# Optimization experiments

Hardware: AMD Instinct MI355X
Metric: run time of the kernel (lower is better)

The kernel has to match this reference:

```python
import jax, jax.numpy as jnp
import numpy as np

B, S, E, H = 2, 2048, 1024, 16
HD = E // H


def setup_inputs() -> dict:
    key = jax.random.key(0)
    ks = jax.random.split(key, 5)
    scale = 1.0 / np.sqrt(E)
    return {
        "x": jax.random.normal(ks[0], (B, S, E), dtype=jnp.float32),
        "Wq": jax.random.normal(ks[1], (H, HD, E), dtype=jnp.float32) * scale,
        "Wk": jax.random.normal(ks[2], (H, HD, E), dtype=jnp.float32) * scale,
        "Wv": jax.random.normal(ks[3], (H, HD, E), dtype=jnp.float32) * scale,
        "Wo": jax.random.normal(ks[4], (E, E), dtype=jnp.float32) * scale,
    }


def reference(x, Wq, Wk, Wv, Wo):
    # Batched per-head projections: torch Linear y = x @ W.T, W: [head_dim, E]
    q = jnp.einsum("bse,hde->bshd", x, Wq)  # [B,S,H,HD]
    k = jnp.einsum("bse,hde->bshd", x, Wk)
    v = jnp.einsum("bse,hde->bshd", x, Wv)
    # Scaled dot-product attention; original scales by sqrt(head_dim)
    scores = jnp.einsum("bqhd,bkhd->bhqk", q, k) / jnp.sqrt(jnp.float32(HD))
    attn = jax.nn.softmax(scores, axis=-1)  # [B,H,S,S]
    out_h = jnp.einsum("bhqk,bkhd->bqhd", attn, v)  # [B,S,H,HD]
    out_cat = out_h.reshape(x.shape[0], x.shape[1], -1)  # concat heads -> [B,S,E]
    return out_cat @ Wo.T
```

## Files before the change

### kernel.cpp

```cpp
#include <hip/hip_runtime.h>
#include <hip/hip_bf16.h>

typedef unsigned short u16;
typedef unsigned int u32;
typedef __attribute__((ext_vector_type(4))) float f32x4;
typedef __attribute__((ext_vector_type(8))) short short8;
typedef __attribute__((ext_vector_type(8))) unsigned short u16x8;
typedef __attribute__((ext_vector_type(4))) unsigned short u16x4;
typedef __attribute__((ext_vector_type(2))) unsigned int u32x2;

#define BATCH 2
#define SEQ   2048
#define EMB   1024
#define NH    16
#define HD    64

__device__ inline u16 f2bf(float f) {
    unsigned u = __builtin_bit_cast(unsigned, f);
    unsigned r = u + 0x7FFFu + ((u >> 16) & 1u);
    return (u16)(r >> 16);
}

__device__ inline float fexp2(float x) {
    float r;
    asm("v_exp_f32 %0, %1" : "=v"(r) : "v"(x));
    return r;
}

__device__ inline void gload16(const void* g, void* l) {
    __builtin_amdgcn_global_load_lds(
        (const __attribute__((address_space(1))) unsigned int*)g,
        (__attribute__((address_space(3))) unsigned int*)l, 16, 0, 0);
}

__global__ __launch_bounds__(256) void convert_all(
    const float* __restrict__ x,
    const float* __restrict__ Wq, const float* __restrict__ Wk, const float* __restrict__ Wv,
    u16* __restrict__ Xb, u16* __restrict__ Wqkv)
{
    const long gidx = (long)blockIdx.x * 2048 + (long)threadIdx.x * 8;
    const float* src;
    u16* dst;
    if (gidx < 4194304L) {
        src = x + gidx; dst = Xb + gidx;
    } else {
        const long r = gidx - 4194304L;
        const int w = (int)(r >> 20);
        const long off = r & 1048575L;
        src = (w == 0 ? Wq : w == 1 ? Wk : Wv) + off;
        dst = Wqkv + r;
    }
    f32x4 a = *(const f32x4*)src;
    f32x4 b = *(const f32x4*)(src + 4);
    u16x8 o;
    #pragma unroll
    for (int j = 0; j < 4; ++j) { o[j] = f2bf(a[j]); o[4 + j] = f2bf(b[j]); }
    *(u16x8*)dst = o;
}

__global__ __launch_bounds__(256) void convert_wo(
    const float* __restrict__ Wo, u16* __restrict__ Wob)
{
    const long gidx = (long)blockIdx.x * 2048 + (long)threadIdx.x * 8;
    f32x4 a = *(const f32x4*)(Wo + gidx);
    f32x4 b = *(const f32x4*)(Wo + gidx + 4);
    u16x8 o;
    #pragma unroll
    for (int j = 0; j < 4; ++j) { o[j] = f2bf(a[j]); o[4 + j] = f2bf(b[j]); }
    *(u16x8*)(Wob + gidx) = o;
}

__global__ __launch_bounds__(512, 2) void gemm256(
    const u16* __restrict__ A, const u16* __restrict__ Bb,
    u16* __restrict__ Qo, u16* __restrict__ Ko, u16* __restrict__ VTo)
{
    __shared__ u16 As[2][256 * 64];
    __shared__ u16 Bs[2][256 * 64];

    const int tid = threadIdx.x;
    const int lane = tid & 63;
    const int wid = tid >> 6;
    const int lr = lane & 15;
    const int lg = lane >> 4;
    const int wr = wid >> 2;
    const int wc = wid & 3;

    const int lin = blockIdx.y * 16 + blockIdx.x;
    const int swz = (lin & 7) * 24 + (lin >> 3);
    const int m0 = (swz & 15) * 256;
    const int n0 = (swz >> 4) * 256;

    const int grow = lane >> 3;
    const int schunk = ((lane & 7) ^ grow) << 4;

    auto issueTile = [&](int kt, int buf) {
        const int k0b = kt * 128;
        #pragma unroll
        for (int i = 0; i < 4; ++i) {
            const int row = i * 64 + wid * 8 + grow;
            gload16((const char*)A + (size_t)(m0 + row) * 2048 + k0b + schunk,
                    (char*)As[buf] + i * 8192 + wid * 1024);
            gload16((const char*)Bb + (size_t)(n0 + row) * 2048 + k0b + schunk,
                    (char*)Bs[buf] + i * 8192 + wid * 1024);
        }
    };

    issueTile(0, 0);
    issueTile(1, 1);

    f32x4 acc[8][4] = {};
    const int rsw = (lr & 7);

    for (int t = 0; t < 16; ++t) {
        if (t < 15) { asm volatile("s_waitcnt vmcnt(8)" ::: "memory"); }
        else        { asm volatile("s_waitcnt vmcnt(0)" ::: "memory"); }
        __builtin_amdgcn_sched_barrier(0);
        __builtin_amdgcn_s_barrier();
        __builtin_amdgcn_sched_barrier(0);

        const u16* Ac = As[t & 1];
        const u16* Bc = Bs[t & 1];

        short8 a[4][2], b0[2][2], b1[2][2];

        #pragma unroll
        for (int fi = 0; fi < 4; ++fi)
            #pragma unroll
            for (int ks = 0; ks < 2; ++ks)
                a[fi][ks] = *(const short8*)((const char*)Ac + (wr * 128 + fi * 16 + lr) * 128
                                             + (((ks * 4 + lg) ^ rsw) << 4));
        #pragma unroll
        for (int fj = 0; fj < 2; ++fj)
            #pragma unroll
            for (int ks = 0; ks < 2; ++ks)
                b0[fj][ks] = *(const short8*)((const char*)Bc + (wc * 64 + fj * 16 + lr) * 128
                                              + (((ks * 4 + lg) ^ rsw) << 4));
        __builtin_amdgcn_s_setprio(1);
        #pragma unroll
        for (int fi = 0; fi < 4; ++fi)
            #pragma unroll
            for (int fj = 0; fj < 2; ++fj)
                #pragma unroll
                for (int ks = 0; ks < 2; ++ks)
                    acc[fi][fj] = __builtin_amdgcn_mfma_f32_16x16x32_bf16(a[fi][ks], b0[fj][ks], acc[fi][fj], 0, 0, 0);
        __builtin_amdgcn_s_setprio(0);

        #pragma unroll
        for (int fj = 0; fj < 2; ++fj)
            #pragma unroll
            for (int ks = 0; ks < 2; ++ks)
                b1[fj][ks] = *(const short8*)((const char*)Bc + (wc * 64 + (fj + 2) * 16 + lr) * 128
                                              + (((ks * 4 + lg) ^ rsw) << 4));
        __builtin_amdgcn_s_setprio(1);
        #pragma unroll
        for (int fi = 0; fi < 4; ++fi)
            #pragma unroll
            for (int fj = 0; fj < 2; ++fj)
                #pragma unroll
                for (int ks = 0; ks < 2; ++ks)
                    acc[fi][fj + 2] = __builtin_amdgcn_mfma_f32_16x16x32_bf16(a[fi][ks], b1[fj][ks], acc[fi][fj + 2], 0, 0, 0);
        __builtin_amdgcn_s_setprio(0);

        #pragma unroll
        for (int fi = 0; fi < 4; ++fi)
            #pragma unroll
            for (int ks = 0; ks < 2; ++ks)
                a[fi][ks] = *(const short8*)((const char*)Ac + (wr * 128 + (fi + 4) * 16 + lr) * 128
                                             + (((ks * 4 + lg) ^ rsw) << 4));
        __builtin_amdgcn_s_setprio(1);
        #pragma unroll
        for (int fi = 0; fi < 4; ++fi)
            #pragma unroll
            for (int fj = 0; fj < 2; ++fj)
                #pragma unroll
                for (int ks = 0; ks < 2; ++ks)
                    acc[fi + 4][fj + 2] = __builtin_amdgcn_mfma_f32_16x16x32_bf16(a[fi][ks], b1[fj][ks], acc[fi + 4][fj + 2], 0, 0, 0);
        __builtin_amdgcn_s_setprio(0);

        __builtin_amdgcn_s_setprio(1);
        #pragma unroll
        for (int fi = 0; fi < 4; ++fi)
            #pragma unroll
            for (int fj = 0; fj < 2; ++fj)
                #pragma unroll
                for (int ks = 0; ks < 2; ++ks)
                    acc[fi + 4][fj] = __builtin_amdgcn_mfma_f32_16x16x32_bf16(a[fi][ks], b0[fj][ks], acc[fi + 4][fj], 0, 0, 0);
        __builtin_amdgcn_s_setprio(0);

        __builtin_amdgcn_sched_barrier(0);
        __builtin_amdgcn_s_barrier();
        __builtin_amdgcn_sched_barrier(0);
        if (t + 2 < 16) issueTile(t + 2, t & 1);
    }

    const int w = n0 >> 10;
    const float qs = (w == 0) ? 0.125f * 1.44269504f : 1.0f;
    const int mb = m0 + wr * 128;
    const int nb = n0 + wc * 64;
    #pragma unroll
    for (int fi = 0; fi < 8; ++fi) {
        #pragma unroll
        for (int fj = 0; fj < 4; ++fj) {
            const int m = mb + fi * 16 + lg * 4;
            const int nn = (nb + fj * 16 + lr) & 1023;
            const int h = nn >> 6, d = nn & 63;
            const int bb = m >> 11, s = m & 2047;
            const size_t bh = (size_t)(bb * NH + h);
            if (w == 2) {
                u16x4 v;
                #pragma unroll
                for (int i = 0; i < 4; ++i) v[i] = f2bf(acc[fi][fj][i]);
                *(u16x4*)&VTo[(bh * HD + d) * SEQ + s] = v;
            } else {
                u16* P = (w == 0) ? Qo : Ko;
                #pragma unroll
                for (int i = 0; i < 4; ++i)
                    P[(bh * SEQ + s + i) * HD + d] = f2bf(acc[fi][fj][i] * qs);
            }
        }
    }
}

__global__ __launch_bounds__(256) void gemm_out(
    const u16* __restrict__ A, const u16* __restrict__ Bb, float* __restrict__ Fo)
{
    __shared__ u16 As[2][128 * 64];
    __shared__ u16 Bs[2][128 * 64];

    const int tid = threadIdx.x;
    const int m0 = blockIdx.x * 128;
    const int n0 = blockIdx.y * 128;

    const int lane = tid & 63;
    const int lr = lane & 15;
    const int lg = lane >> 4;
    const int wid = tid >> 6;
    const int wm = wid >> 1, wn = wid & 1;

    const int grow = lane >> 3;
    const int gcolb = ((lane & 7) ^ grow) << 4;
    const int rswz = (lr & 7);

    f32x4 acc[4][4] = {};

    auto issue = [&](int kt, int buf) {
        const int k0b = kt * 128;
        #pragma unroll
        for (int t = 0; t < 4; ++t) {
            const int row = (wid * 4 + t) * 8 + grow;
            gload16((const char*)A + (size_t)(m0 + row) * 2048 + k0b + gcolb,
                    (char*)As[buf] + (wid * 4 + t) * 1024);
            gload16((const char*)Bb + (size_t)(n0 + row) * 2048 + k0b + gcolb,
                    (char*)Bs[buf] + (wid * 4 + t) * 1024);
        }
    };

    issue(0, 0);
    issue(1, 1);

    for (int kt = 0; kt < 16; ++kt) {
        if (kt < 15) { asm volatile("s_waitcnt vmcnt(8)" ::: "memory"); }
        else         { asm volatile("s_waitcnt vmcnt(0)" ::: "memory"); }
        __builtin_amdgcn_sched_barrier(0);
        __builtin_amdgcn_s_barrier();
        __builtin_amdgcn_sched_barrier(0);

        const u16* Ac = As[kt & 1];
        const u16* Bc = Bs[kt & 1];
        #pragma unroll
        for (int kk = 0; kk < 2; ++kk) {
            short8 a[4], b[4];
            #pragma unroll
            for (int i = 0; i < 4; ++i)
                a[i] = *(const short8*)((const char*)Ac + (wm * 64 + i * 16 + lr) * 128
                                        + (((kk * 4 + lg) ^ rswz) << 4));
            #pragma unroll
            for (int i = 0; i < 4; ++i)
                b[i] = *(const short8*)((const char*)Bc + (wn * 64 + i * 16 + lr) * 128
                                        + (((kk * 4 + lg) ^ rswz) << 4));
            #pragma unroll
            for (int mi = 0; mi < 4; ++mi)
                #pragma unroll
                for (int ni = 0; ni < 4; ++ni)
                    acc[mi][ni] = __builtin_amdgcn_mfma_f32_16x16x32_bf16(a[mi], b[ni], acc[mi][ni], 0, 0, 0);
        }

        __builtin_amdgcn_sched_barrier(0);
        __builtin_amdgcn_s_barrier();
        __builtin_amdgcn_sched_barrier(0);
        if (kt + 2 < 16) issue(kt + 2, kt & 1);
    }

    const int mb = m0 + wm * 64;
    const int nb = n0 + wn * 64;
    #pragma unroll
    for (int mi = 0; mi < 4; ++mi)
        #pragma unroll
        for (int ni = 0; ni < 4; ++ni) {
            const int m = mb + mi * 16 + lg * 4;
            const int n = nb + ni * 16 + lr;
            #pragma unroll
            for (int i = 0; i < 4; ++i)
                Fo[(size_t)(m + i) * EMB + n] = acc[mi][ni][i];
        }
}

__global__ __launch_bounds__(512) void attn_fwd(
    const u16* __restrict__ Q, const u16* __restrict__ K,
    const u16* __restrict__ VT, u16* __restrict__ Cat)
{
    __shared__ u16 Ks[2][64 * 64];
    __shared__ u16 Vs[2][80 * 64];
    __shared__ u16 PT[8][16 * 72];

    const int tid = threadIdx.x;
    const int lane = tid & 63;
    const int lr = lane & 15;
    const int lg = lane >> 4;
    const int wid = tid >> 6;

    const int lin = blockIdx.y * 16 + blockIdx.x;
    const int swz = (lin & 7) * 64 + (lin >> 3);
    const int qt = swz & 15;
    const int bh = swz >> 4;
    const int b = bh >> 4, h = bh & 15;

    if (tid < 128) {
        const int row = 64 + (tid >> 3), sl = tid & 7;
        u16x8 ones;
        #pragma unroll
        for (int j = 0; j < 8; ++j) ones[j] = 0x3F80;
        *(u16x8*)((char*)Vs[0] + row * 128 + ((sl ^ (row & 7)) << 4)) = ones;
        *(u16x8*)((char*)Vs[1] + row * 128 + ((sl ^ (row & 7)) << 4)) = ones;
    }
    asm volatile("s_waitcnt lgkmcnt(0)" ::: "memory");

    const u16* Qg = Q + ((size_t)bh * SEQ + qt * 128 + wid * 16 + lr) * HD;
    short8 qf[2];
    qf[0] = *(const short8*)(Qg + lg * 8);
    qf[1] = *(const short8*)(Qg + 32 + lg * 8);

    float m = -1e30f;
    f32x4 accO[5] = {};

    const u16* Kg = K + (size_t)bh * SEQ * HD;
    const u16* Vg = VT + (size_t)bh * HD * SEQ;

    const int srow = lane >> 3;
    const int schunk = ((lane & 7) ^ srow) << 4;

    auto issueKV = [&](int nt, int buf) {
        const int kv0 = nt * 64;
        const int krow = wid * 8 + srow;
        gload16((const char*)Kg + (size_t)(kv0 + krow) * 128 + schunk,
                (char*)Ks[buf] + wid * 1024);
        gload16((const char*)Vg + (size_t)krow * (SEQ * 2) + kv0 * 2 + schunk,
                (char*)Vs[buf] + wid * 1024);
    };

    issueKV(0, 0);
    issueKV(1, 1);

    const int NT = SEQ / 64;
    for (int nt = 0; nt < NT; ++nt) {
        const int cur = nt & 1;
        if (nt < NT - 1) { asm volatile("s_waitcnt vmcnt(2)" ::: "memory"); }
        else             { asm volatile("s_waitcnt vmcnt(0)" ::: "memory"); }
        __builtin_amdgcn_sched_barrier(0);
        __builtin_amdgcn_s_barrier();
        __builtin_amdgcn_sched_barrier(0);

        f32x4 st[4] = {};
        #pragma unroll
        for (int kk = 0; kk < 2; ++kk) {
            const short8 qv = qf[kk];
            #pragma unroll
            for (int c = 0; c < 4; ++c) {
                const short8 kf = *(const short8*)((const char*)Ks[cur] + (c * 16 + lr) * 128
                                                   + (((kk * 4 + lg) ^ (lr & 7)) << 4));
                st[c] = __builtin_amdgcn_mfma_f32_16x16x32_bf16(kf, qv, st[c], 0, 0, 0);
            }
        }

        float mx = fmaxf(
            fmaxf(fmaxf(fmaxf(st[0][0], st[0][1]), fmaxf(st[0][2], st[0][3])),
                  fmaxf(fmaxf(st[1][0], st[1][1]), fmaxf(st[1][2], st[1][3]))),
            fmaxf(fmaxf(fmaxf(st[2][0], st[2][1]), fmaxf(st[2][2], st[2][3])),
                  fmaxf(fmaxf(st[3][0], st[3][1]), fmaxf(st[3][2], st[3][3]))));
        mx = fmaxf(mx, __shfl_xor(mx, 16));
        mx = fmaxf(mx, __shfl_xor(mx, 32));
        if (!__all(mx - m <= 11.5f)) {
            const float nm = fmaxf(m, mx);
            const float corr = fexp2(m - nm);
            m = nm;
            #pragma unroll
            for (int dc = 0; dc < 5; ++dc)
                accO[dc] *= corr;
        }
        #pragma unroll
        for (int c = 0; c < 4; ++c)
            #pragma unroll
            for (int i = 0; i < 4; ++i)
                st[c][i] = fexp2(st[c][i] - m);

        #pragma unroll
        for (int c = 0; c < 4; ++c) {
            u32 w0, w1;
            asm("v_cvt_pk_bf16_f32 %0, %1, %2" : "=v"(w0) : "v"(st[c][0]), "v"(st[c][1]));
            asm("v_cvt_pk_bf16_f32 %0, %1, %2" : "=v"(w1) : "v"(st[c][2]), "v"(st[c][3]));
            u32x2 pk; pk[0] = w0; pk[1] = w1;
            *(u32x2*)&PT[wid][lr * 72 + c * 16 + lg * 4] = pk;
        }
        asm volatile("s_waitcnt lgkmcnt(0)" ::: "memory");
        __builtin_amdgcn_sched_barrier(0);

        #pragma unroll
        for (int kk = 0; kk < 2; ++kk) {
            const short8 pf = *(const short8*)&PT[wid][lr * 72 + kk * 32 + lg * 8];
            #pragma unroll
            for (int dc = 0; dc < 5; ++dc) {
                const short8 vf = *(const short8*)((const char*)Vs[cur] + (dc * 16 + lr) * 128
                                                   + (((kk * 4 + lg) ^ (lr & 7)) << 4));
                accO[dc] = __builtin_amdgcn_mfma_f32_16x16x32_bf16(vf, pf, accO[dc], 0, 0, 0);
            }
        }

        __builtin_amdgcn_sched_barrier(0);
        __builtin_amdgcn_s_barrier();
        __builtin_amdgcn_sched_barrier(0);
        if (nt + 2 < NT) issueKV(nt + 2, cur);
    }

    const float invl = 1.f / accO[4][0];
    const int qs = qt * 128 + wid * 16 + lr;
    u16* ob = Cat + (size_t)b * SEQ * EMB + (size_t)qs * EMB + h * HD;
    #pragma unroll
    for (int dc = 0; dc < 4; ++dc) {
        u16x4 o;
        #pragma unroll
        for (int i = 0; i < 4; ++i) o[i] = f2bf(accO[dc][i] * invl);
        *(u16x4*)&ob[dc * 16 + lg * 4] = o;
    }
}

extern "C" void kernel_launch(void* const* d_in, const int* in_sizes, int n_in,
                              void* d_out, int out_size, void* d_ws, size_t ws_size,
                              hipStream_t stream) {
    const float* x  = (const float*)d_in[0];
    const float* Wq = (const float*)d_in[1];
    const float* Wk = (const float*)d_in[2];
    const float* Wv = (const float*)d_in[3];
    const float* Wo = (const float*)d_in[4];
    float* out = (float*)d_out;

    u16* Xb   = (u16*)d_out;
    u16* Wqkv = (u16*)d_out + (size_t)4 * 1048576;

    char* ws = (char*)d_ws;
    u16* Qb  = (u16*)(ws);
    u16* Kb  = (u16*)(ws + (size_t)8  * 1048576);
    u16* VTb = (u16*)(ws + (size_t)16 * 1048576);
    u16* Cat = (u16*)(ws + (size_t)24 * 1048576);
    u16* Wob = Qb;

    convert_all<<<3584, 256, 0, stream>>>(x, Wq, Wk, Wv, Xb, Wqkv);

    dim3 g1(4096 / 256, 3072 / 256);
    gemm256<<<g1, 512, 0, stream>>>(Xb, Wqkv, Qb, Kb, VTb);

    dim3 g2(SEQ / 128, BATCH * NH);
    attn_fwd<<<g2, 512, 0, stream>>>(Qb, Kb, VTb, Cat);

    convert_wo<<<512, 256, 0, stream>>>(Wo, Wob);
    dim3 g3(4096 / 128, 1024 / 128);
    gemm_out<<<g3, 256, 0, stream>>>(Cat, Wob, out);
}
```

Measured before the change: 126.2 us.

## Software-pipeline PV matmul behind next QK tile; swizzle output GEMM blocks

The attention loop now runs the P·V MFMAs for the previous KV tile right after the current tile's QK^T MFMAs. This lets softmax exp work and the two MFMA chains overlap, and drops one workgroup barrier per iteration. V staging grows to four LDS buffers so the delayed PV read does not collide with incoming prefetches, at the cost of extra LDS and one epilogue PV step. Separately, the output projection GEMM remaps block indices with a grouped swizzle, so blocks running at the same time share A/B tiles in L2.

```diff
diff --git a/kernel.cpp b/kernel.cpp
--- a/kernel.cpp
+++ b/kernel.cpp
@@ -228,8 +228,11 @@
     __shared__ u16 Bs[2][128 * 64];
 
     const int tid = threadIdx.x;
-    const int m0 = blockIdx.x * 128;
-    const int n0 = blockIdx.y * 128;
+
+    const int lin = blockIdx.y * 32 + blockIdx.x;
+    const int swz = (lin & 7) * 32 + (lin >> 3);
+    const int m0 = (swz & 31) * 128;
+    const int n0 = (swz >> 5) * 128;
 
     const int lane = tid & 63;
     const int lr = lane & 15;
@@ -310,7 +313,7 @@
     const u16* __restrict__ VT, u16* __restrict__ Cat)
 {
     __shared__ u16 Ks[2][64 * 64];
-    __shared__ u16 Vs[2][80 * 64];
+    __shared__ u16 Vs[4][80 * 64];
     __shared__ u16 PT[8][16 * 72];
 
     const int tid = threadIdx.x;
@@ -330,8 +333,10 @@
         u16x8 ones;
         #pragma unroll
         for (int j = 0; j < 8; ++j) ones[j] = 0x3F80;
-        *(u16x8*)((char*)Vs[0] + row * 128 + ((sl ^ (row & 7)) << 4)) = ones;
-        *(u16x8*)((char*)Vs[1] + row * 128 + ((sl ^ (row & 7)) << 4)) = ones;
+        const int off = row * 128 + ((sl ^ (row & 7)) << 4);
+        #pragma unroll
+        for (int bf = 0; bf < 4; ++bf)
+            *(u16x8*)((char*)Vs[bf] + off) = ones;
     }
     asm volatile("s_waitcnt lgkmcnt(0)" ::: "memory");
 
@@ -349,17 +354,17 @@
     const int srow = lane >> 3;
     const int schunk = ((lane & 7) ^ srow) << 4;
 
-    auto issueKV = [&](int nt, int buf) {
+    auto issueKV = [&](int nt) {
         const int kv0 = nt * 64;
         const int krow = wid * 8 + srow;
         gload16((const char*)Kg + (size_t)(kv0 + krow) * 128 + schunk,
-                (char*)Ks[buf] + wid * 1024);
+                (char*)Ks[nt & 1] + wid * 1024);
         gload16((const char*)Vg + (size_t)krow * (SEQ * 2) + kv0 * 2 + schunk,
-                (char*)Vs[buf] + wid * 1024);
+                (char*)Vs[nt & 3] + wid * 1024);
     };
 
-    issueKV(0, 0);
-    issueKV(1, 1);
+    issueKV(0);
+    issueKV(1);
 
     const int NT = SEQ / 64;
     for (int nt = 0; nt < NT; ++nt) {
@@ -379,6 +384,20 @@
                 const short8 kf = *(const short8*)((const char*)Ks[cur] + (c * 16 + lr) * 128
                                                    + (((kk * 4 + lg) ^ (lr & 7)) << 4));
                 st[c] = __builtin_amdgcn_mfma_f32_16x16x32_bf16(kf, qv, st[c], 0, 0, 0);
+            }
+        }
+
+        if (nt > 0) {
+            const char* Vp = (const char*)Vs[(nt - 1) & 3];
+            #pragma unroll
+            for (int kk = 0; kk < 2; ++kk) {
+                const short8 pf = *(const short8*)&PT[wid][lr * 72 + kk * 32 + lg * 8];
+                #pragma unroll
+                for (int dc = 0; dc < 5; ++dc) {
+                    const short8 vf = *(const short8*)(Vp + (dc * 16 + lr) * 128
+                                                       + (((kk * 4 + lg) ^ (lr & 7)) << 4));
+                    accO[dc] = __builtin_amdgcn_mfma_f32_16x16x32_bf16(vf, pf, accO[dc], 0, 0, 0);
+                }
             }
         }
 
@@ -414,21 +433,23 @@
         asm volatile("s_waitcnt lgkmcnt(0)" ::: "memory");
         __builtin_amdgcn_sched_barrier(0);
 
+        __builtin_amdgcn_s_barrier();
+        __builtin_amdgcn_sched_barrier(0);
+        if (nt + 2 < NT) issueKV(nt + 2);
+    }
+
+    {
+        const char* Vp = (const char*)Vs[(NT - 1) & 3];
         #pragma unroll
         for (int kk = 0; kk < 2; ++kk) {
             const short8 pf = *(const short8*)&PT[wid][lr * 72 + kk * 32 + lg * 8];
             #pragma unroll
             for (int dc = 0; dc < 5; ++dc) {
-                const short8 vf = *(const short8*)((const char*)Vs[cur] + (dc * 16 + lr) * 128
+                const short8 vf = *(const short8*)(Vp + (dc * 16 + lr) * 128
                                                    + (((kk * 4 + lg) ^ (lr & 7)) << 4));
                 accO[dc] = __builtin_amdgcn_mfma_f32_16x16x32_bf16(vf, pf, accO[dc], 0, 0, 0);
             }
         }
-
-        __builtin_amdgcn_sched_barrier(0);
-        __builtin_amdgcn_s_barrier();
-        __builtin_amdgcn_sched_barrier(0);
-        if (nt + 2 < NT) issueKV(nt + 2, cur);
     }
 
     const float invl = 1.f / accO[4][0];
```

Result: no change. 128.1 us (+1.6%).

## Rewrite attention with 32x32 MFMA and register-resident P via permlane swaps

Applied to the files above, without the earlier changes.

The attention kernel moves from 16x16x32 to 32x32x16 bf16 MFMA with 32 query rows per wave and 256 per block. The probability tile is kept in registers using v_permlane32_swap instead of going through a shared-memory PT buffer. The row sum is now computed explicitly rather than through an extra ones-row in V. The output GEMM also gets a block-index swizzle for L2 locality. The aim is to cut LDS traffic and waits and raise MFMA efficiency, at the cost of more registers per wave and half as many attention blocks.

```diff
diff --git a/kernel.cpp b/kernel.cpp
--- a/kernel.cpp
+++ b/kernel.cpp
@@ -4,10 +4,11 @@
 typedef unsigned short u16;
 typedef unsigned int u32;
 typedef __attribute__((ext_vector_type(4))) float f32x4;
+typedef __attribute__((ext_vector_type(16))) float f32x16;
 typedef __attribute__((ext_vector_type(8))) short short8;
 typedef __attribute__((ext_vector_type(8))) unsigned short u16x8;
 typedef __attribute__((ext_vector_type(4))) unsigned short u16x4;
-typedef __attribute__((ext_vector_type(2))) unsigned int u32x2;
+typedef __attribute__((ext_vector_type(4))) unsigned int u32x4;
 
 #define BATCH 2
 #define SEQ   2048
@@ -32,6 +33,27 @@
         (const __attribute__((address_space(1))) unsigned int*)g,
         (__attribute__((address_space(3))) unsigned int*)l, 16, 0, 0);
 }
+
+__device__ inline short8 mk8(u32 a, u32 b, u32 c, u32 d) {
+    u32x4 t; t[0] = a; t[1] = b; t[2] = c; t[3] = d;
+    return __builtin_bit_cast(short8, t);
+}
+
+#define PACK_ST(st, w0,w1,w2,w3,w4,w5,w6,w7)                                   \
+  {                                                                            \
+    asm("v_cvt_pk_bf16_f32 %0, %1, %2" : "=v"(w0) : "v"(st[0]),  "v"(st[1]));  \
+    asm("v_cvt_pk_bf16_f32 %0, %1, %2" : "=v"(w1) : "v"(st[2]),  "v"(st[3]));  \
+    asm("v_cvt_pk_bf16_f32 %0, %1, %2" : "=v"(w2) : "v"(st[4]),  "v"(st[5]));  \
+    asm("v_cvt_pk_bf16_f32 %0, %1, %2" : "=v"(w3) : "v"(st[6]),  "v"(st[7]));  \
+    asm("v_permlane32_swap_b32 %0, %1" : "+v"(w0), "+v"(w2));                  \
+    asm("v_permlane32_swap_b32 %0, %1" : "+v"(w1), "+v"(w3));                  \
+    asm("v_cvt_pk_bf16_f32 %0, %1, %2" : "=v"(w4) : "v"(st[8]),  "v"(st[9]));  \
+    asm("v_cvt_pk_bf16_f32 %0, %1, %2" : "=v"(w5) : "v"(st[10]), "v"(st[11])); \
+    asm("v_cvt_pk_bf16_f32 %0, %1, %2" : "=v"(w6) : "v"(st[12]), "v"(st[13])); \
+    asm("v_cvt_pk_bf16_f32 %0, %1, %2" : "=v"(w7) : "v"(st[14]), "v"(st[15])); \
+    asm("v_permlane32_swap_b32 %0, %1" : "+v"(w4), "+v"(w6));                  \
+    asm("v_permlane32_swap_b32 %0, %1" : "+v"(w5), "+v"(w7));                  \
+  }
 
 __global__ __launch_bounds__(256) void convert_all(
     const float* __restrict__ x,
@@ -228,8 +250,11 @@
     __shared__ u16 Bs[2][128 * 64];
 
     const int tid = threadIdx.x;
-    const int m0 = blockIdx.x * 128;
-    const int n0 = blockIdx.y * 128;
+
+    const int lin = blockIdx.y * 32 + blockIdx.x;
+    const int swz = (lin & 7) * 32 + (lin >> 3);
+    const int m0 = (swz & 31) * 128;
+    const int n0 = (swz >> 5) * 128;
 
     const int lane = tid & 63;
     const int lr = lane & 15;
@@ -310,38 +335,28 @@
     const u16* __restrict__ VT, u16* __restrict__ Cat)
 {
     __shared__ u16 Ks[2][64 * 64];
-    __shared__ u16 Vs[2][80 * 64];
-    __shared__ u16 PT[8][16 * 72];
+    __shared__ u16 Vs[2][64 * 64];
 
     const int tid = threadIdx.x;
     const int lane = tid & 63;
-    const int lr = lane & 15;
-    const int lg = lane >> 4;
     const int wid = tid >> 6;
-
-    const int lin = blockIdx.y * 16 + blockIdx.x;
-    const int swz = (lin & 7) * 64 + (lin >> 3);
-    const int qt = swz & 15;
-    const int bh = swz >> 4;
+    const int lq = lane & 31;
+    const int hi = lane >> 5;
+
+    const int lin = blockIdx.y * 8 + blockIdx.x;
+    const int swz = (lin & 7) * 32 + (lin >> 3);
+    const int qt = swz & 7;
+    const int bh = swz >> 3;
     const int b = bh >> 4, h = bh & 15;
 
-    if (tid < 128) {
-        const int row = 64 + (tid >> 3), sl = tid & 7;
-        u16x8 ones;
-        #pragma unroll
-        for (int j = 0; j < 8; ++j) ones[j] = 0x3F80;
-        *(u16x8*)((char*)Vs[0] + row * 128 + ((sl ^ (row & 7)) << 4)) = ones;
-        *(u16x8*)((char*)Vs[1] + row * 128 + ((sl ^ (row & 7)) << 4)) = ones;
-    }
-    asm volatile("s_waitcnt lgkmcnt(0)" ::: "memory");
-
-    const u16* Qg = Q + ((size_t)bh * SEQ + qt * 128 + wid * 16 + lr) * HD;
-    short8 qf[2];
-    qf[0] = *(const short8*)(Qg + lg * 8);
-    qf[1] = *(const short8*)(Qg + 32 + lg * 8);
-
-    float m = -1e30f;
-    f32x4 accO[5] = {};
+    const u16* Qg = Q + ((size_t)bh * SEQ + qt * 256 + wid * 32 + lq) * HD;
+    short8 qf[4];
+    #pragma unroll
+    for (int ks = 0; ks < 4; ++ks)
+        qf[ks] = *(const short8*)((const char*)Qg + ks * 32 + hi * 16);
+
+    float m = -1e30f, l = 0.f;
+    f32x16 ot0 = {}, ot1 = {};
 
     const u16* Kg = K + (size_t)bh * SEQ * HD;
     const u16* Vg = VT + (size_t)bh * HD * SEQ;
@@ -349,18 +364,19 @@
     const int srow = lane >> 3;
     const int schunk = ((lane & 7) ^ srow) << 4;
 
-    auto issueKV = [&](int nt, int buf) {
+    auto issueKV = [&](int nt) {
         const int kv0 = nt * 64;
         const int krow = wid * 8 + srow;
         gload16((const char*)Kg + (size_t)(kv0 + krow) * 128 + schunk,
-                (char*)Ks[buf] + wid * 1024);
+                (char*)Ks[nt & 1] + wid * 1024);
         gload16((const char*)Vg + (size_t)krow * (SEQ * 2) + kv0 * 2 + schunk,
-                (char*)Vs[buf] + wid * 1024);
+                (char*)Vs[nt & 1] + wid * 1024);
     };
 
-    issueKV(0, 0);
-    issueKV(1, 1);
-
+    issueKV(0);
+    issueKV(1);
+
+    const int rsw = (lq & 7);
     const int NT = SEQ / 64;
     for (int nt = 0; nt < NT; ++nt) {
         const int cur = nt & 1;
@@ -370,76 +386,77 @@
         __builtin_amdgcn_s_barrier();
         __builtin_amdgcn_sched_barrier(0);
 
-        f32x4 st[4] = {};
-        #pragma unroll
-        for (int kk = 0; kk < 2; ++kk) {
-            const short8 qv = qf[kk];
-            #pragma unroll
-            for (int c = 0; c < 4; ++c) {
-                const short8 kf = *(const short8*)((const char*)Ks[cur] + (c * 16 + lr) * 128
-                                                   + (((kk * 4 + lg) ^ (lr & 7)) << 4));
-                st[c] = __builtin_amdgcn_mfma_f32_16x16x32_bf16(kf, qv, st[c], 0, 0, 0);
-            }
-        }
-
-        float mx = fmaxf(
-            fmaxf(fmaxf(fmaxf(st[0][0], st[0][1]), fmaxf(st[0][2], st[0][3])),
-                  fmaxf(fmaxf(st[1][0], st[1][1]), fmaxf(st[1][2], st[1][3]))),
-            fmaxf(fmaxf(fmaxf(st[2][0], st[2][1]), fmaxf(st[2][2], st[2][3])),
-                  fmaxf(fmaxf(st[3][0], st[3][1]), fmaxf(st[3][2], st[3][3]))));
-        mx = fmaxf(mx, __shfl_xor(mx, 16));
+        f32x16 st0 = {}, st1 = {};
+        #pragma unroll
+        for (int ks = 0; ks < 4; ++ks) {
+            const int co = ((ks * 2 + hi) ^ rsw) << 4;
+            const short8 kf0 = *(const short8*)((const char*)Ks[cur] + lq * 128 + co);
+            const short8 kf1 = *(const short8*)((const char*)Ks[cur] + (32 + lq) * 128 + co);
+            st0 = __builtin_amdgcn_mfma_f32_32x32x16_bf16(kf0, qf[ks], st0, 0, 0, 0);
+            st1 = __builtin_amdgcn_mfma_f32_32x32x16_bf16(kf1, qf[ks], st1, 0, 0, 0);
+        }
+
+        float mx = st0[0];
+        #pragma unroll
+        for (int i = 1; i < 16; ++i) mx = fmaxf(mx, st0[i]);
+        #pragma unroll
+        for (int i = 0; i < 16; ++i) mx = fmaxf(mx, st1[i]);
         mx = fmaxf(mx, __shfl_xor(mx, 32));
         if (!__all(mx - m <= 11.5f)) {
             const float nm = fmaxf(m, mx);
             const float corr = fexp2(m - nm);
             m = nm;
-            #pragma unroll
-            for (int dc = 0; dc < 5; ++dc)
-                accO[dc] *= corr;
-        }
-        #pragma unroll
-        for (int c = 0; c < 4; ++c)
-            #pragma unroll
-            for (int i = 0; i < 4; ++i)
-                st[c][i] = fexp2(st[c][i] - m);
-
-        #pragma unroll
-        for (int c = 0; c < 4; ++c) {
-            u32 w0, w1;
-            asm("v_cvt_pk_bf16_f32 %0, %1, %2" : "=v"(w0) : "v"(st[c][0]), "v"(st[c][1]));
-            asm("v_cvt_pk_bf16_f32 %0, %1, %2" : "=v"(w1) : "v"(st[c][2]), "v"(st[c][3]));
-            u32x2 pk; pk[0] = w0; pk[1] = w1;
-            *(u32x2*)&PT[wid][lr * 72 + c * 16 + lg * 4] = pk;
-        }
-        asm volatile("s_waitcnt lgkmcnt(0)" ::: "memory");
-        __builtin_amdgcn_sched_barrier(0);
-
-        #pragma unroll
-        for (int kk = 0; kk < 2; ++kk) {
-            const short8 pf = *(const short8*)&PT[wid][lr * 72 + kk * 32 + lg * 8];
-            #pragma unroll
-            for (int dc = 0; dc < 5; ++dc) {
-                const short8 vf = *(const short8*)((const char*)Vs[cur] + (dc * 16 + lr) * 128
-                                                   + (((kk * 4 + lg) ^ (lr & 7)) << 4));
-                accO[dc] = __builtin_amdgcn_mfma_f32_16x16x32_bf16(vf, pf, accO[dc], 0, 0, 0);
-            }
-        }
-
-        __builtin_amdgcn_sched_barrier(0);
-        __builtin_amdgcn_s_barrier();
-        __builtin_amdgcn_sched_barrier(0);
-        if (nt + 2 < NT) issueKV(nt + 2, cur);
-    }
-
-    const float invl = 1.f / accO[4][0];
-    const int qs = qt * 128 + wid * 16 + lr;
-    u16* ob = Cat + (size_t)b * SEQ * EMB + (size_t)qs * EMB + h * HD;
-    #pragma unroll
-    for (int dc = 0; dc < 4; ++dc) {
-        u16x4 o;
-        #pragma unroll
-        for (int i = 0; i < 4; ++i) o[i] = f2bf(accO[dc][i] * invl);
-        *(u16x4*)&ob[dc * 16 + lg * 4] = o;
+            l *= corr;
+            #pragma unroll
+            for (int i = 0; i < 16; ++i) { ot0[i] *= corr; ot1[i] *= corr; }
+        }
+        float rs = 0.f;
+        #pragma unroll
+        for (int i = 0; i < 16; ++i) {
+            st0[i] = fexp2(st0[i] - m); rs += st0[i];
+            st1[i] = fexp2(st1[i] - m); rs += st1[i];
+        }
+        rs += __shfl_xor(rs, 32);
+        l += rs;
+
+        u32 a0, a1, a2, a3, a4, a5, a6, a7;
+        u32 c0, c1, c2, c3, c4, c5, c6, c7;
+        PACK_ST(st0, a0, a1, a2, a3, a4, a5, a6, a7);
+        PACK_ST(st1, c0, c1, c2, c3, c4, c5, c6, c7);
+        const short8 pf0 = mk8(a0, a1, a2, a3);
+        const short8 pf1 = mk8(a4, a5, a6, a7);
+        const short8 pf2 = mk8(c0, c1, c2, c3);
+        const short8 pf3 = mk8(c4, c5, c6, c7);
+
+        #pragma unroll
+        for (int ks = 0; ks < 4; ++ks) {
+            const short8 pf = (ks == 0) ? pf0 : (ks == 1) ? pf1 : (ks == 2) ? pf2 : pf3;
+            const int co = ((ks * 2 + hi) ^ rsw) << 4;
+            const short8 vf0 = *(const short8*)((const char*)Vs[cur] + lq * 128 + co);
+            const short8 vf1 = *(const short8*)((const char*)Vs[cur] + (32 + lq) * 128 + co);
+            ot0 = __builtin_amdgcn_mfma_f32_32x32x16_bf16(vf0, pf, ot0, 0, 0, 0);
+            ot1 = __builtin_amdgcn_mfma_f32_32x32x16_bf16(vf1, pf, ot1, 0, 0, 0);
+        }
+
+        __builtin_amdgcn_sched_barrier(0);
+        __builtin_amdgcn_s_barrier();
+        __builtin_amdgcn_sched_barrier(0);
+        if (nt + 2 < NT) issueKV(nt + 2);
+    }
+
+    const float invl = 1.f / l;
+    const int qrow = qt * 256 + wid * 32 + lq;
+    u16* ob = Cat + ((size_t)b * SEQ + qrow) * EMB + h * HD;
+    #pragma unroll
+    for (int g = 0; g < 4; ++g) {
+        u16x4 o0, o1;
+        #pragma unroll
+        for (int i = 0; i < 4; ++i) {
+            o0[i] = f2bf(ot0[g * 4 + i] * invl);
+            o1[i] = f2bf(ot1[g * 4 + i] * invl);
+        }
+        *(u16x4*)&ob[g * 8 + hi * 4] = o0;
+        *(u16x4*)&ob[32 + g * 8 + hi * 4] = o1;
     }
 }
 
@@ -468,7 +485,7 @@
     dim3 g1(4096 / 256, 3072 / 256);
     gemm256<<<g1, 512, 0, stream>>>(Xb, Wqkv, Qb, Kb, VTb);
 
-    dim3 g2(SEQ / 128, BATCH * NH);
+    dim3 g2(SEQ / 256, BATCH * NH);
     attn_fwd<<<g2, 512, 0, stream>>>(Qb, Kb, VTb, Cat);
 
     convert_wo<<<512, 256, 0, stream>>>(Wo, Wob);
```

Result: slower. 129.0 us (+2.3%).
